# Optimization experiments

Measured on AMD Instinct MI355X. Metric: run time of the kernel, lower is better.

Reference implementation:

```python
import jax, jax.numpy as jnp
import numpy as np

HIDDEN = 2048
CHANNELS = 4096      # in_channels == out_channels
KERNEL = 4
GROUPS = 4096        # depthwise conv


def setup_inputs() -> dict:
    key = jax.random.key(0)
    k = jax.random.split(key, 7)
    std = 0.02
    inp = {
        "hidden_states": jax.random.normal(k[0], (4, 4096, HIDDEN), dtype=jnp.float32),
        "w_in": jax.random.normal(k[1], (CHANNELS, HIDDEN), dtype=jnp.float32) * std,
        "b_in": jnp.zeros((CHANNELS,), dtype=jnp.float32),
        # grouped conv kernel: [out_channels, in_channels // groups, kernel]
        "conv_w": jax.random.normal(k[2], (CHANNELS, CHANNELS // GROUPS, KERNEL), dtype=jnp.float32) * std,
        "conv_b": jnp.zeros((CHANNELS,), dtype=jnp.float32),
        "w_out": jax.random.normal(k[3], (HIDDEN, CHANNELS), dtype=jnp.float32) * std,
        "b_out": jnp.zeros((HIDDEN,), dtype=jnp.float32),
    }
    return inp


def reference(hidden_states, w_in, b_in, conv_w, conv_b, w_out, b_out):
    # input projection: [B,S,H] @ [H,C]^T -> [B,S,C]
    x = jnp.einsum("bsh,ch->bsc", hidden_states, w_in) + b_in
    # causal depthwise conv1d: torch Conv1d(padding=K-1) cropped to first S
    # positions == left-pad (K-1) causal conv.
    x = jnp.transpose(x, (0, 2, 1))  # [B,C,S]
    x = jax.lax.conv_general_dilated(
        x, conv_w,
        window_strides=(1,),
        padding=[(KERNEL - 1, 0)],
        dimension_numbers=("NCH", "OIH", "NCH"),
        feature_group_count=GROUPS,
    ) + conv_b[None, :, None]
    x = jax.nn.silu(x)
    x = jnp.transpose(x, (0, 2, 1))  # [B,S,C]
    # output projection: [B,S,C] @ [C,H]^T -> [B,S,H]
    return jnp.einsum("bsc,hc->bsh", x, w_out) + b_out
```

## Files before the change

kernel.cpp:

```cpp
#include <hip/hip_runtime.h>
#include <hip/hip_bf16.h>
#include <stdint.h>

#define SEQ      4096
#define BATCH    4
#define HIDDEN   2048
#define CHANNELS 4096
#define MTOT     (BATCH*SEQ)

typedef __bf16 bf16;
typedef __bf16 bf16x8 __attribute__((ext_vector_type(8)));
typedef float  f32x4  __attribute__((ext_vector_type(4)));

#define GLDS16(g, l) __builtin_amdgcn_global_load_lds(                      \
    (const __attribute__((address_space(1))) void*)(g),                     \
    (__attribute__((address_space(3))) void*)(l), 16, 0, 0)

union B8 { uint4 v; bf16 h[8]; };

#define SBAR() do {                                   \
    __builtin_amdgcn_sched_barrier(0);                \
    __builtin_amdgcn_s_barrier();                     \
    asm volatile("" ::: "memory");                    \
    __builtin_amdgcn_sched_barrier(0); } while (0)
#define LGKM0() do {                                  \
    asm volatile("s_waitcnt lgkmcnt(0)" ::: "memory");\
    __builtin_amdgcn_sched_barrier(0); } while (0)

__global__ __launch_bounds__(256)
void cast_f32_to_bf16(const float* __restrict__ in, bf16* __restrict__ out) {
    const long long i = (long long)blockIdx.x * 256 + threadIdx.x;
    const float4 a = ((const float4*)in)[2 * i];
    const float4 b = ((const float4*)in)[2 * i + 1];
    B8 o;
    o.h[0] = (bf16)a.x; o.h[1] = (bf16)a.y; o.h[2] = (bf16)a.z; o.h[3] = (bf16)a.w;
    o.h[4] = (bf16)b.x; o.h[5] = (bf16)b.y; o.h[6] = (bf16)b.z; o.h[7] = (bf16)b.w;
    *(uint4*)(out + 8 * i) = o.v;
}

template <typename OutT, int N, int K>
__global__ __launch_bounds__(512, 2)
void gemm256_bt_bias(const bf16* __restrict__ A, const bf16* __restrict__ B,
                     const float* __restrict__ bias, OutT* __restrict__ C) {
    constexpr int NT    = K / 64;
    constexpr int NTILE = N / 256;
    __shared__ bf16 lds[8][128 * 64];

    const int tid  = threadIdx.x;
    const int lane = tid & 63;
    const int wave = tid >> 6;
    const int wr   = wave >> 2;
    const int wc   = wave & 3;
    const int quad = lane >> 4;
    const int lrow = lane & 15;

    const int nwg = gridDim.x;
    const int bid = blockIdx.x;
    const int swz = (bid & 7) * (nwg >> 3) + (bid >> 3);
    const int ni  = swz % NTILE;
    const int mi  = swz / NTILE;
    const long long bm = (long long)mi * 256;
    const long long bn = (long long)ni * 256;

    f32x4 acc[2][2][4][2] = {};
    bf16x8 a[4][2], b0[2][2], b1[2][2];

    auto STAGE = [&](int s) {
        const int kind = s & 3;
        const int slot = s & 7;
        const int kt   = (s >> 2) * 64;
        const bf16* src = (kind & 1) ? B : A;
        const long long rbase = ((kind & 1) ? bn : bm) + (long long)(kind >> 1) * 128;
#pragma unroll
        for (int r = 0; r < 2; ++r) {
            const int c   = tid + r * 512;
            const int row = c >> 3;
            const int qg  = (c & 7) ^ (row & 7);
            GLDS16(src + (rbase + row) * K + (kt + qg * 8),
                   (char*)lds[slot] + c * 16);
        }
    };
    auto READ_A = [&](bf16x8 (&dst)[4][2], int bufb, int mh) {
#pragma unroll
        for (int i = 0; i < 4; ++i) {
            const int rl = wr * 64 + i * 16 + lrow;
            const bf16* base = &lds[bufb + mh * 2][rl * 64];
#pragma unroll
            for (int h = 0; h < 2; ++h)
                dst[i][h] = *(const bf16x8*)(base + ((h * 4 + quad) ^ (rl & 7)) * 8);
        }
    };
    auto READ_B = [&](bf16x8 (&dst)[2][2], int bufb, int nh) {
#pragma unroll
        for (int j = 0; j < 2; ++j) {
            const int rl = wc * 32 + j * 16 + lrow;
            const bf16* base = &lds[bufb + nh * 2 + 1][rl * 64];
#pragma unroll
            for (int h = 0; h < 2; ++h)
                dst[j][h] = *(const bf16x8*)(base + ((h * 4 + quad) ^ (rl & 7)) * 8);
        }
    };
    auto MFMAQ = [&](int mh, int nh, bf16x8 (&Af)[4][2], bf16x8 (&Bf)[2][2]) {
        __builtin_amdgcn_s_setprio(1);
#pragma unroll
        for (int h = 0; h < 2; ++h)
#pragma unroll
            for (int i = 0; i < 4; ++i)
#pragma unroll
                for (int j = 0; j < 2; ++j)
                    acc[mh][nh][i][j] = __builtin_amdgcn_mfma_f32_16x16x32_bf16(
                        Af[i][h], Bf[j][h], acc[mh][nh][i][j], 0, 0, 0);
        __builtin_amdgcn_s_setprio(0);
    };

#pragma unroll
    for (int s = 0; s < 6; ++s) STAGE(s);
    asm volatile("s_waitcnt vmcnt(4)" ::: "memory");
    SBAR();

    for (int T = 0; T < NT; ++T) {
        const int bufb = (T & 1) * 4;
        const int P0   = 4 * T;

        READ_A(a, bufb, 0);
        READ_B(b0, bufb, 0);
        if (P0 + 6 < 4 * NT) STAGE(P0 + 6);
        SBAR(); LGKM0();
        MFMAQ(0, 0, a, b0);
        SBAR();

        READ_B(b1, bufb, 1);
        if (P0 + 7 < 4 * NT) STAGE(P0 + 7);
        SBAR(); LGKM0();
        MFMAQ(0, 1, a, b1);
        SBAR();

        READ_A(a, bufb, 1);
        if (P0 + 8 < 4 * NT) STAGE(P0 + 8);
        SBAR(); LGKM0();
        MFMAQ(1, 1, a, b1);
        SBAR();

        if (P0 + 9 < 4 * NT) STAGE(P0 + 9);
        SBAR();
        MFMAQ(1, 0, a, b0);
        if (T < NT - 2)       asm volatile("s_waitcnt vmcnt(4)" ::: "memory");
        else if (T == NT - 2) asm volatile("s_waitcnt vmcnt(0)" ::: "memory");
        SBAR();
    }

#pragma unroll
    for (int nh = 0; nh < 2; ++nh)
#pragma unroll
        for (int j = 0; j < 2; ++j) {
            const long long gcol = bn + nh * 128 + wc * 32 + j * 16 + lrow;
            const float bv = bias[gcol];
#pragma unroll
            for (int mh = 0; mh < 2; ++mh)
#pragma unroll
                for (int i = 0; i < 4; ++i) {
                    const long long grow0 = bm + mh * 128 + wr * 64 + i * 16 + quad * 4;
#pragma unroll
                    for (int r = 0; r < 4; ++r)
                        C[(grow0 + r) * N + gcol] = (OutT)(acc[mh][nh][i][j][r] + bv);
                }
        }
}

__global__ __launch_bounds__(256)
void conv_silu_kernel(const bf16* __restrict__ X, const float* __restrict__ cw,
                      const float* __restrict__ cb, bf16* __restrict__ Y) {
    const int gid = blockIdx.x * 256 + threadIdx.x;
    const int c0  = (gid & 511) << 3;
    const long long bs0 = (long long)(gid >> 9) * 8;
    const int s0  = (int)(bs0 & (SEQ - 1));

    float w[8][4];
#pragma unroll
    for (int j = 0; j < 8; ++j) {
        const float4 t = *(const float4*)(cw + (long long)(c0 + j) * 4);
        w[j][0] = t.x; w[j][1] = t.y; w[j][2] = t.z; w[j][3] = t.w;
    }
    float bv[8];
    {
        const float4 b0 = *(const float4*)(cb + c0);
        const float4 b1 = *(const float4*)(cb + c0 + 4);
        bv[0] = b0.x; bv[1] = b0.y; bv[2] = b0.z; bv[3] = b0.w;
        bv[4] = b1.x; bv[5] = b1.y; bv[6] = b1.z; bv[7] = b1.w;
    }

    B8 rows[11];
#pragma unroll
    for (int t = 0; t < 11; ++t) {
        if (s0 + t - 3 >= 0)
            rows[t].v = *(const uint4*)(X + (bs0 + t - 3) * CHANNELS + c0);
        else
            rows[t].v = uint4{0, 0, 0, 0};
    }

#pragma unroll
    for (int t = 0; t < 8; ++t) {
        B8 o;
#pragma unroll
        for (int j = 0; j < 8; ++j) {
            float a = bv[j];
            a += w[j][0] * (float)rows[t + 0].h[j];
            a += w[j][1] * (float)rows[t + 1].h[j];
            a += w[j][2] * (float)rows[t + 2].h[j];
            a += w[j][3] * (float)rows[t + 3].h[j];
            o.h[j] = (bf16)(a / (1.0f + __expf(-a)));
        }
        *(uint4*)(Y + (bs0 + t) * CHANNELS + c0) = o.v;
    }
}

extern "C" void kernel_launch(void* const* d_in, const int* in_sizes, int n_in,
                              void* d_out, int out_size, void* d_ws, size_t ws_size,
                              hipStream_t stream) {
    const float* hs    = (const float*)d_in[0];
    const float* w_in  = (const float*)d_in[1];
    const float* b_in  = (const float*)d_in[2];
    const float* cw    = (const float*)d_in[3];
    const float* cb    = (const float*)d_in[4];
    const float* w_out = (const float*)d_in[5];
    const float* b_out = (const float*)d_in[6];
    float* out = (float*)d_out;

    char* ws = (char*)d_ws;
    bf16* X       = (bf16*)(ws);
    bf16* Y       = (bf16*)(ws + ((size_t)128 << 20));
    bf16* hs_b    = (bf16*)(ws + ((size_t)128 << 20));
    bf16* w_in_b  = (bf16*)(ws + ((size_t)192 << 20));
    bf16* w_out_b = (bf16*)(ws + ((size_t)256 << 20));

    cast_f32_to_bf16<<<(MTOT * HIDDEN) / (8 * 256), 256, 0, stream>>>(hs, hs_b);
    cast_f32_to_bf16<<<(CHANNELS * HIDDEN) / (8 * 256), 256, 0, stream>>>(w_in, w_in_b);
    cast_f32_to_bf16<<<(HIDDEN * CHANNELS) / (8 * 256), 256, 0, stream>>>(w_out, w_out_b);

    gemm256_bt_bias<bf16, CHANNELS, HIDDEN>
        <<<(MTOT / 256) * (CHANNELS / 256), 512, 0, stream>>>(hs_b, w_in_b, b_in, X);

    conv_silu_kernel<<<(MTOT / 8) * (CHANNELS / 8) / 256, 256, 0, stream>>>(X, cw, cb, Y);

    gemm256_bt_bias<float, HIDDEN, CHANNELS>
        <<<(MTOT / 256) * (HIDDEN / 256), 512, 0, stream>>>(Y, w_out_b, b_out, out);
}
```

Baseline: 795.2 us.

## Software-pipeline LDS fragment reads with MFMA using ping-pong registers

Restructures the GEMM main loop so that LDS reads for the next quadrant, and for the next K-tile's first A/B fragments, are issued while the current MFMA block runs. The explicit lgkmcnt(0) waits go away, and a separate barrier before each MFMA block is dropped. The loop is unrolled by two with ping-pong register sets, and the last two iterations are specialised at compile time to drop the bounds checks on stage issue. This raises register pressure at 2 waves/SIMD launch bounds and relies on compiler-inserted waits for the LDS reads.

```diff
diff --git a/kernel.cpp b/kernel.cpp
--- a/kernel.cpp
+++ b/kernel.cpp
@@ -18,13 +18,15 @@
 
 union B8 { uint4 v; bf16 h[8]; };
 
+template <int M> struct IC { static constexpr int value = M; };
+
 #define SBAR() do {                                   \
     __builtin_amdgcn_sched_barrier(0);                \
     __builtin_amdgcn_s_barrier();                     \
     asm volatile("" ::: "memory");                    \
     __builtin_amdgcn_sched_barrier(0); } while (0)
-#define LGKM0() do {                                  \
-    asm volatile("s_waitcnt lgkmcnt(0)" ::: "memory");\
+#define VMCNT(n) do {                                 \
+    asm volatile("s_waitcnt vmcnt(" #n ")" ::: "memory"); \
     __builtin_amdgcn_sched_barrier(0); } while (0)
 
 __global__ __launch_bounds__(256)
@@ -63,7 +65,8 @@
     const long long bn = (long long)ni * 256;
 
     f32x4 acc[2][2][4][2] = {};
-    bf16x8 a[4][2], b0[2][2], b1[2][2];
+    bf16x8 a0A[4][2], a0B[4][2];
+    bf16x8 b0A[2][2], b0B[2][2];
 
     auto STAGE = [&](int s) {
         const int kind = s & 3;
@@ -80,25 +83,19 @@
                    (char*)lds[slot] + c * 16);
         }
     };
-    auto READ_A = [&](bf16x8 (&dst)[4][2], int bufb, int mh) {
-#pragma unroll
-        for (int i = 0; i < 4; ++i) {
-            const int rl = wr * 64 + i * 16 + lrow;
-            const bf16* base = &lds[bufb + mh * 2][rl * 64];
-#pragma unroll
-            for (int h = 0; h < 2; ++h)
-                dst[i][h] = *(const bf16x8*)(base + ((h * 4 + quad) ^ (rl & 7)) * 8);
-        }
-    };
-    auto READ_B = [&](bf16x8 (&dst)[2][2], int bufb, int nh) {
-#pragma unroll
-        for (int j = 0; j < 2; ++j) {
-            const int rl = wc * 32 + j * 16 + lrow;
-            const bf16* base = &lds[bufb + nh * 2 + 1][rl * 64];
-#pragma unroll
-            for (int h = 0; h < 2; ++h)
-                dst[j][h] = *(const bf16x8*)(base + ((h * 4 + quad) ^ (rl & 7)) * 8);
-        }
+    auto RD_A = [&](bf16x8 (&dst)[4][2], int slot, int i) {
+        const int rl = wr * 64 + i * 16 + lrow;
+        const bf16* base = &lds[slot][rl * 64];
+#pragma unroll
+        for (int h = 0; h < 2; ++h)
+            dst[i][h] = *(const bf16x8*)(base + ((h * 4 + quad) ^ (rl & 7)) * 8);
+    };
+    auto RD_B = [&](bf16x8 (&dst)[2][2], int slot, int j) {
+        const int rl = wc * 32 + j * 16 + lrow;
+        const bf16* base = &lds[slot][rl * 64];
+#pragma unroll
+        for (int h = 0; h < 2; ++h)
+            dst[j][h] = *(const bf16x8*)(base + ((h * 4 + quad) ^ (rl & 7)) * 8);
     };
     auto MFMAQ = [&](int mh, int nh, bf16x8 (&Af)[4][2], bf16x8 (&Bf)[2][2]) {
         __builtin_amdgcn_s_setprio(1);
@@ -113,41 +110,61 @@
         __builtin_amdgcn_s_setprio(0);
     };
 
+    auto BODY = [&](int T, auto modeTag,
+                    bf16x8 (&a0c)[4][2], bf16x8 (&b0c)[2][2],
+                    bf16x8 (&a0n)[4][2], bf16x8 (&b0n)[2][2]) {
+        constexpr int MODE = decltype(modeTag)::value;
+        const int bufb = (T & 1) * 4;
+        const int nbuf = bufb ^ 4;
+        const int P0   = 4 * T;
+        bf16x8 a1[4][2], b1[2][2];
+
+        RD_B(b1, bufb + 3, 0); RD_B(b1, bufb + 3, 1);
+        RD_A(a1, bufb + 2, 0);
+        if constexpr (MODE <= 1) STAGE(P0 + 6);
+        MFMAQ(0, 0, a0c, b0c);
+        SBAR();
+
+        RD_A(a1, bufb + 2, 1); RD_A(a1, bufb + 2, 2); RD_A(a1, bufb + 2, 3);
+        if constexpr (MODE <= 1) STAGE(P0 + 7);
+        MFMAQ(0, 1, a0c, b1);
+        if constexpr (MODE <= 1) VMCNT(6);
+        SBAR();
+
+        if constexpr (MODE != 2) {
+            RD_A(a0n, nbuf + 0, 0); RD_A(a0n, nbuf + 0, 1); RD_A(a0n, nbuf + 0, 2);
+        }
+        if constexpr (MODE == 0) STAGE(P0 + 8);
+        MFMAQ(1, 1, a1, b1);
+        if constexpr (MODE == 0) { VMCNT(6); }
+        else if constexpr (MODE == 1) { VMCNT(4); }
+        SBAR();
+
+        if constexpr (MODE != 2) {
+            RD_A(a0n, nbuf + 0, 3);
+            RD_B(b0n, nbuf + 1, 0); RD_B(b0n, nbuf + 1, 1);
+        }
+        if constexpr (MODE == 0) STAGE(P0 + 9);
+        MFMAQ(1, 0, a1, b0c);
+        if constexpr (MODE == 0) { VMCNT(4); }
+        else if constexpr (MODE == 1) { VMCNT(0); }
+        SBAR();
+    };
+
 #pragma unroll
     for (int s = 0; s < 6; ++s) STAGE(s);
-    asm volatile("s_waitcnt vmcnt(4)" ::: "memory");
+    VMCNT(4);
     SBAR();
-
-    for (int T = 0; T < NT; ++T) {
-        const int bufb = (T & 1) * 4;
-        const int P0   = 4 * T;
-
-        READ_A(a, bufb, 0);
-        READ_B(b0, bufb, 0);
-        if (P0 + 6 < 4 * NT) STAGE(P0 + 6);
-        SBAR(); LGKM0();
-        MFMAQ(0, 0, a, b0);
-        SBAR();
-
-        READ_B(b1, bufb, 1);
-        if (P0 + 7 < 4 * NT) STAGE(P0 + 7);
-        SBAR(); LGKM0();
-        MFMAQ(0, 1, a, b1);
-        SBAR();
-
-        READ_A(a, bufb, 1);
-        if (P0 + 8 < 4 * NT) STAGE(P0 + 8);
-        SBAR(); LGKM0();
-        MFMAQ(1, 1, a, b1);
-        SBAR();
-
-        if (P0 + 9 < 4 * NT) STAGE(P0 + 9);
-        SBAR();
-        MFMAQ(1, 0, a, b0);
-        if (T < NT - 2)       asm volatile("s_waitcnt vmcnt(4)" ::: "memory");
-        else if (T == NT - 2) asm volatile("s_waitcnt vmcnt(0)" ::: "memory");
-        SBAR();
-    }
+#pragma unroll
+    for (int i = 0; i < 4; ++i) RD_A(a0A, 0, i);
+    RD_B(b0A, 1, 0); RD_B(b0A, 1, 1);
+
+    for (int T = 0; T < NT - 2; T += 2) {
+        BODY(T,     IC<0>{}, a0A, b0A, a0B, b0B);
+        BODY(T + 1, IC<0>{}, a0B, b0B, a0A, b0A);
+    }
+    BODY(NT - 2, IC<1>{}, a0A, b0A, a0B, b0B);
+    BODY(NT - 1, IC<2>{}, a0B, b0B, a0A, b0A);
 
 #pragma unroll
     for (int nh = 0; nh < 2; ++nh)
```

New measurement: 1.282 ms. 1.61x slower.
